# Kernel optimization log

Measured on AMD Instinct MI355X. Metric: run time of the kernel, lower is better.

## Reference

```python
import jax, jax.numpy as jnp
import numpy as np

N, C, H, W = 8, 192, 112, 112
TEMPERATURE = 0.1


def setup_inputs() -> dict:
    key = jax.random.key(0)
    k1, k2 = jax.random.split(key)
    features = jax.random.normal(k1, (N, C, H, W), dtype=jnp.float32)
    # Raw per-pixel directions in {-1, 0, 1}; clip the neighbor coordinate into
    # bounds and recompute the direction so EVERY neighbor is valid. The torch
    # module's broadcasting (labels[:, i, j] vs an (N, M) gather) only works when
    # all N neighbors are valid at each pixel, so this matches its assumptions.
    raw = jax.random.randint(k2, (N, 2, H, W), -1, 2)
    ii = jnp.arange(H)[None, :, None]
    jj = jnp.arange(W)[None, None, :]
    d0 = jnp.clip(ii + raw[:, 0], 0, H - 1) - ii
    d1 = jnp.clip(jj + raw[:, 1], 0, W - 1) - jj
    directions = jnp.stack([d0, d1], axis=1).astype(jnp.int32)
    # Single-class labels: the original loss is -inf whenever any mask entry is 0
    # (log of exactly 0), so a finite, comparable baseline needs matching labels.
    labels = jnp.zeros((N, H, W), dtype=jnp.int32)
    return {"features": features, "labels": labels, "directions": directions}


def reference(features, labels, directions):
    # F.normalize(features, dim=1): x / max(||x||_2, eps)
    norm = jnp.linalg.norm(features, axis=1, keepdims=True)
    fn = features / jnp.maximum(norm, 1e-12)

    ii = jnp.arange(H)[None, :, None]
    jj = jnp.arange(W)[None, None, :]
    ni = ii + directions[:, 0]  # (N, H, W), in-bounds by construction
    nj = jj + directions[:, 1]  # (N, H, W)

    # Torch: features[:, :, neighbor_i, neighbor_j] gathers the M(==N) neighbor
    # coordinates across ALL batch elements -> (N, C, N, H, W) = [n, c, m, i, j]
    gathered = fn[:, :, ni, nj]
    # logits[n, m, i, j] = <fn[n, :, i, j], fn[n, :, ni[m,i,j], nj[m,i,j]]> / T
    logits = jnp.einsum('ncij,ncmij->nmij', fn, gathered) / TEMPERATURE

    # mask[n, m, i, j] = (labels[m, i, j] == labels[n, ni[m,i,j], nj[m,i,j]])
    # (torch broadcasts labels[:, i, j] along the first axis of the (N, M) gather)
    labels_g = labels[:, ni, nj]  # (N, N, H, W) = [n, m, i, j]
    mask = (labels[None, :, :, :] == labels_g).astype(fn.dtype)

    exp_l = jnp.exp(logits) * mask
    denom = jnp.sum(exp_l, axis=1, keepdims=True)  # sum over m
    # sum_{i,j} mean_{n,m}(.) / (H*W) == global mean over (n, m, i, j)
    loss = (-jnp.log(exp_l / (denom + 1e-6))).mean()
    return loss
```

## Files before the change

### kernel.cpp

```cpp
#include <hip/hip_runtime.h>
#include <math.h>


namespace {
constexpr int N_ = 8, C_ = 192, H_ = 112, W_ = 112;
constexpr int HW = H_ * W_;
constexpr int TH = 2;
constexpr int WS = 56;
constexpr int TROWS = TH + 2;
constexpr int TCOLS = WS + 2;
constexpr int TILE_E = TROWS * TCOLS;
constexpr int NT = 128;
constexpr int NPX = TH * WS;
constexpr int EXTRA = TILE_E - NT;
constexpr int KCH = 8;
constexpr int GRP = KCH / 2;
constexpr int NCHUNK = C_ / KCH;
constexpr int NBLK = 2 * (H_ / TH) * N_;
constexpr float INV_T = 10.0f;
constexpr double TOTAL = (double)N_ * N_ * H_ * W_;
}

__device__ __forceinline__ float sel3(int d, float a, float b, float c) {
    float r = (d < 0) ? a : b;
    return (d > 0) ? c : r;
}

extern "C" __global__ void __launch_bounds__(NT, 4)
dcl_main(const float* __restrict__ feat,
         const int* __restrict__ labels,
         const int* __restrict__ dirs,
         double* __restrict__ partial, int use_partial)
{
    __shared__ float2 tiles[2][GRP][TILE_E];
    __shared__ float ssbuf[TILE_E];
    __shared__ float red[NT / 64];

    const int tid = threadIdx.x;
    const int gx0 = blockIdx.x * WS;
    const int gy0 = blockIdx.y * TH;
    const int n   = blockIdx.z;

    int gofs0, gofs1 = 0;
    {
        int r = tid / TCOLS, c = tid - r * TCOLS;
        gofs0 = min(max(gy0 + r - 1, 0), H_ - 1) * W_ + min(max(gx0 + c - 1, 0), W_ - 1);
        if (tid < EXTRA) {
            int t2 = tid + NT;
            r = t2 / TCOLS; c = t2 - r * TCOLS;
            gofs1 = min(max(gy0 + r - 1, 0), H_ - 1) * W_ + min(max(gx0 + c - 1, 0), W_ - 1);
        }
    }

    const bool is_px = (tid < NPX);
    const int ty = tid / WS;
    const int tx = tid - ty * WS;
    const int gi = gy0 + ty;
    const int gj = gx0 + tx;
    const int ci = (ty + 1) * TCOLS + (tx + 1);

    const float* __restrict__ plane = feat + (size_t)n * C_ * HW;

    float ss0 = 0.0f, ss1 = 0.0f;

    {
        #pragma unroll
        for (int g = 0; g < GRP; ++g) {
            float v0 = plane[(size_t)(2 * g) * HW + gofs0];
            float v1 = plane[(size_t)(2 * g + 1) * HW + gofs0];
            ss0 += v0 * v0 + v1 * v1;
            tiles[0][g][tid] = make_float2(v0, v1);
        }
        if (tid < EXTRA) {
            #pragma unroll
            for (int g = 0; g < GRP; ++g) {
                float u0 = plane[(size_t)(2 * g) * HW + gofs1];
                float u1 = plane[(size_t)(2 * g + 1) * HW + gofs1];
                ss1 += u0 * u0 + u1 * u1;
                tiles[0][g][tid + NT] = make_float2(u0, u1);
            }
        }
    }
    __syncthreads();

    float s[9];
    #pragma unroll
    for (int d = 0; d < 9; ++d) s[d] = 0.0f;

    for (int t = 0; t < NCHUNK; ++t) {
        float pv0[KCH], pv1[KCH];
        const bool more = (t + 1 < NCHUNK);
        if (more) {
            const float* p = plane + (size_t)(t + 1) * KCH * HW;
            #pragma unroll
            for (int k = 0; k < KCH; ++k) pv0[k] = p[(size_t)k * HW + gofs0];
            if (tid < EXTRA) {
                #pragma unroll
                for (int k = 0; k < KCH; ++k) pv1[k] = p[(size_t)k * HW + gofs1];
            }
        }

        if (is_px) {
            #pragma unroll
            for (int g = 0; g < GRP; ++g) {
                const float2* __restrict__ cp = tiles[t & 1][g];
                float2 fc  = cp[ci];
                float2 n00 = cp[ci - TCOLS - 1];
                float2 n01 = cp[ci - TCOLS];
                float2 n02 = cp[ci - TCOLS + 1];
                float2 n10 = cp[ci - 1];
                float2 n12 = cp[ci + 1];
                float2 n20 = cp[ci + TCOLS - 1];
                float2 n21 = cp[ci + TCOLS];
                float2 n22 = cp[ci + TCOLS + 1];
                s[0] = fmaf(fc.x, n00.x, s[0]); s[0] = fmaf(fc.y, n00.y, s[0]);
                s[1] = fmaf(fc.x, n01.x, s[1]); s[1] = fmaf(fc.y, n01.y, s[1]);
                s[2] = fmaf(fc.x, n02.x, s[2]); s[2] = fmaf(fc.y, n02.y, s[2]);
                s[3] = fmaf(fc.x, n10.x, s[3]); s[3] = fmaf(fc.y, n10.y, s[3]);
                s[4] = fmaf(fc.x, fc.x,  s[4]); s[4] = fmaf(fc.y, fc.y,  s[4]);
                s[5] = fmaf(fc.x, n12.x, s[5]); s[5] = fmaf(fc.y, n12.y, s[5]);
                s[6] = fmaf(fc.x, n20.x, s[6]); s[6] = fmaf(fc.y, n20.y, s[6]);
                s[7] = fmaf(fc.x, n21.x, s[7]); s[7] = fmaf(fc.y, n21.y, s[7]);
                s[8] = fmaf(fc.x, n22.x, s[8]); s[8] = fmaf(fc.y, n22.y, s[8]);
            }
        }

        if (more) {
            #pragma unroll
            for (int g = 0; g < GRP; ++g) {
                float v0 = pv0[2 * g], v1 = pv0[2 * g + 1];
                ss0 += v0 * v0 + v1 * v1;
                tiles[(t + 1) & 1][g][tid] = make_float2(v0, v1);
            }
            if (tid < EXTRA) {
                #pragma unroll
                for (int g = 0; g < GRP; ++g) {
                    float u0 = pv1[2 * g], u1 = pv1[2 * g + 1];
                    ss1 += u0 * u0 + u1 * u1;
                    tiles[(t + 1) & 1][g][tid + NT] = make_float2(u0, u1);
                }
            }
            __syncthreads();
        }
    }

    __syncthreads();
    ssbuf[tid] = 1.0f / fmaxf(sqrtf(ss0), 1e-12f);
    if (tid < EXTRA)
        ssbuf[tid + NT] = 1.0f / fmaxf(sqrtf(ss1), 1e-12f);
    __syncthreads();

    float lp = 0.0f;
    if (is_px) {
        const float invc = ssbuf[ci] * INV_T;
        const float l00 = s[0] * invc * ssbuf[ci - TCOLS - 1];
        const float l01 = s[1] * invc * ssbuf[ci - TCOLS];
        const float l02 = s[2] * invc * ssbuf[ci - TCOLS + 1];
        const float l10 = s[3] * invc * ssbuf[ci - 1];
        const float l11 = s[4] * invc * ssbuf[ci];
        const float l12 = s[5] * invc * ssbuf[ci + 1];
        const float l20 = s[6] * invc * ssbuf[ci + TCOLS - 1];
        const float l21 = s[7] * invc * ssbuf[ci + TCOLS];
        const float l22 = s[8] * invc * ssbuf[ci + TCOLS + 1];

        const int pix = gi * W_ + gj;
        float denom = 0.f, sumlog = 0.f;
        #pragma unroll
        for (int m = 0; m < N_; ++m) {
            int d0 = dirs[((m * 2 + 0) * H_ + gi) * W_ + gj];
            int d1 = dirs[((m * 2 + 1) * H_ + gi) * W_ + gj];
            float q0 = sel3(d1, l00, l01, l02);
            float q1 = sel3(d1, l10, l11, l12);
            float q2 = sel3(d1, l20, l21, l22);
            float lm = sel3(d0, q0, q1, q2);
            int labm = labels[m * HW + pix];
            int labn = labels[n * HW + (gi + d0) * W_ + (gj + d1)];
            bool msk = (labm == labn);
            float e = msk ? __expf(lm) : 0.f;
            denom += e;
            sumlog += msk ? lm : -INFINITY;
        }
        lp = 8.0f * __logf(denom + 1e-6f) - sumlog;
    }

    #pragma unroll
    for (int off = 32; off > 0; off >>= 1) lp += __shfl_down(lp, off, 64);
    const int wave = tid >> 6, lane = tid & 63;
    if (lane == 0) red[wave] = lp;
    __syncthreads();
    if (tid == 0) {
        const int bid = (blockIdx.z * gridDim.y + blockIdx.y) * gridDim.x + blockIdx.x;
        float t = red[0] + red[1];
        if (use_partial) partial[bid] = (double)t;
        else atomicAdd(partial, (double)t);
    }
}

extern "C" __global__ void __launch_bounds__(256)
dcl_final(const double* __restrict__ partial, float* __restrict__ out, int nblk)
{
    const int tid = threadIdx.x;
    double s = 0.0;
    for (int i = tid; i < nblk; i += 256) s += partial[i];
    #pragma unroll
    for (int off = 32; off > 0; off >>= 1) s += __shfl_down(s, off, 64);
    __shared__ double red[4];
    const int lane = tid & 63, wv = tid >> 6;
    if (lane == 0) red[wv] = s;
    __syncthreads();
    if (tid == 0) out[0] = (float)((red[0] + red[1] + red[2] + red[3]) / TOTAL);
}

extern "C" void kernel_launch(void* const* d_in, const int* in_sizes, int n_in,
                              void* d_out, int out_size, void* d_ws, size_t ws_size,
                              hipStream_t stream) {
    const float* feat   = (const float*)d_in[0];
    const int*   labels = (const int*)d_in[1];
    const int*   dirs   = (const int*)d_in[2];
    double* acc = (double*)d_ws;
    float*  out = (float*)d_out;

    const int use_partial = (ws_size >= (size_t)NBLK * sizeof(double)) ? 1 : 0;
    if (!use_partial) hipMemsetAsync(acc, 0, sizeof(double), stream);
    dim3 grid(2, H_ / TH, N_);
    dcl_main<<<grid, NT, 0, stream>>>(feat, labels, dirs, acc, use_partial);
    dcl_final<<<1, 256, 0, stream>>>(acc, out, use_partial ? NBLK : 1);
}
```

Before: 127.2 us.

## Split channels across two half-blocks, taller tiles, packed FMA dot products

```diff
diff --git a/kernel.cpp b/kernel.cpp
--- a/kernel.cpp
+++ b/kernel.cpp
@@ -5,20 +5,29 @@
 namespace {
 constexpr int N_ = 8, C_ = 192, H_ = 112, W_ = 112;
 constexpr int HW = H_ * W_;
-constexpr int TH = 2;
+constexpr int TH = 4;
 constexpr int WS = 56;
 constexpr int TROWS = TH + 2;
 constexpr int TCOLS = WS + 2;
 constexpr int TILE_E = TROWS * TCOLS;
-constexpr int NT = 128;
+constexpr int NT2 = 256;
+constexpr int NT = 2 * NT2;
 constexpr int NPX = TH * WS;
-constexpr int EXTRA = TILE_E - NT;
+constexpr int EXTRA = TILE_E - NT2;
+constexpr int CHALF = C_ / 2;
 constexpr int KCH = 8;
-constexpr int GRP = KCH / 2;
-constexpr int NCHUNK = C_ / KCH;
-constexpr int NBLK = 2 * (H_ / TH) * N_;
+constexpr int GRP = KCH / 4;
+constexpr int NCHUNK = CHALF / KCH;
+constexpr int NBLK = (W_ / WS) * (H_ / TH) * N_;
 constexpr float INV_T = 10.0f;
 constexpr double TOTAL = (double)N_ * N_ * H_ * W_;
+}
+
+typedef float v2f __attribute__((ext_vector_type(2)));
+typedef float v4f __attribute__((ext_vector_type(4)));
+
+__device__ __forceinline__ void pkfma(v2f& a, v2f x, v2f y) {
+    asm("v_pk_fma_f32 %0, %1, %2, %0" : "+v"(a) : "v"(x), "v"(y));
 }
 
 __device__ __forceinline__ float sel3(int d, float a, float b, float c) {
@@ -32,60 +41,72 @@
          const int* __restrict__ dirs,
          double* __restrict__ partial, int use_partial)
 {
-    __shared__ float2 tiles[2][GRP][TILE_E];
+    __shared__ v4f   tiles[2][2][GRP][TILE_E];
+    __shared__ float ssp[2][TILE_E];
     __shared__ float ssbuf[TILE_E];
+    __shared__ float scomb[NPX][9];
     __shared__ float red[NT / 64];
 
-    const int tid = threadIdx.x;
+    const int tid  = threadIdx.x;
+    const int half = tid >> 8;
+    const int t8   = tid & (NT2 - 1);
     const int gx0 = blockIdx.x * WS;
     const int gy0 = blockIdx.y * TH;
     const int n   = blockIdx.z;
 
     int gofs0, gofs1 = 0;
     {
-        int r = tid / TCOLS, c = tid - r * TCOLS;
+        int r = t8 / TCOLS, c = t8 - r * TCOLS;
         gofs0 = min(max(gy0 + r - 1, 0), H_ - 1) * W_ + min(max(gx0 + c - 1, 0), W_ - 1);
-        if (tid < EXTRA) {
-            int t2 = tid + NT;
+        if (t8 < EXTRA) {
+            int t2 = t8 + NT2;
             r = t2 / TCOLS; c = t2 - r * TCOLS;
             gofs1 = min(max(gy0 + r - 1, 0), H_ - 1) * W_ + min(max(gx0 + c - 1, 0), W_ - 1);
         }
     }
 
-    const bool is_px = (tid < NPX);
-    const int ty = tid / WS;
-    const int tx = tid - ty * WS;
+    const bool is_px = (t8 < NPX);
+    const int ty = t8 / WS;
+    const int tx = t8 - ty * WS;
     const int gi = gy0 + ty;
     const int gj = gx0 + tx;
     const int ci = (ty + 1) * TCOLS + (tx + 1);
 
-    const float* __restrict__ plane = feat + (size_t)n * C_ * HW;
+    const float* __restrict__ plane =
+        feat + ((size_t)n * C_ + (size_t)half * CHALF) * HW;
 
     float ss0 = 0.0f, ss1 = 0.0f;
 
     {
         #pragma unroll
         for (int g = 0; g < GRP; ++g) {
-            float v0 = plane[(size_t)(2 * g) * HW + gofs0];
-            float v1 = plane[(size_t)(2 * g + 1) * HW + gofs0];
-            ss0 += v0 * v0 + v1 * v1;
-            tiles[0][g][tid] = make_float2(v0, v1);
-        }
-        if (tid < EXTRA) {
+            float a0 = plane[(size_t)(4 * g + 0) * HW + gofs0];
+            float a1 = plane[(size_t)(4 * g + 1) * HW + gofs0];
+            float a2 = plane[(size_t)(4 * g + 2) * HW + gofs0];
+            float a3 = plane[(size_t)(4 * g + 3) * HW + gofs0];
+            ss0 += a0 * a0 + a1 * a1 + a2 * a2 + a3 * a3;
+            v4f v = {a0, a1, a2, a3};
+            tiles[half][0][g][t8] = v;
+        }
+        if (t8 < EXTRA) {
             #pragma unroll
             for (int g = 0; g < GRP; ++g) {
-                float u0 = plane[(size_t)(2 * g) * HW + gofs1];
-                float u1 = plane[(size_t)(2 * g + 1) * HW + gofs1];
-                ss1 += u0 * u0 + u1 * u1;
-                tiles[0][g][tid + NT] = make_float2(u0, u1);
-            }
-        }
-    }
-    __syncthreads();
-
-    float s[9];
+                float a0 = plane[(size_t)(4 * g + 0) * HW + gofs1];
+                float a1 = plane[(size_t)(4 * g + 1) * HW + gofs1];
+                float a2 = plane[(size_t)(4 * g + 2) * HW + gofs1];
+                float a3 = plane[(size_t)(4 * g + 3) * HW + gofs1];
+                ss1 += a0 * a0 + a1 * a1 + a2 * a2 + a3 * a3;
+                v4f v = {a0, a1, a2, a3};
+                tiles[half][0][g][t8 + NT2] = v;
+            }
+        }
+    }
+    __syncthreads();
+
+    v2f s2[9];
+    const v2f zero2 = {0.0f, 0.0f};
     #pragma unroll
-    for (int d = 0; d < 9; ++d) s[d] = 0.0f;
+    for (int d = 0; d < 9; ++d) s2[d] = zero2;
 
     for (int t = 0; t < NCHUNK; ++t) {
         float pv0[KCH], pv1[KCH];
@@ -94,7 +115,7 @@
             const float* p = plane + (size_t)(t + 1) * KCH * HW;
             #pragma unroll
             for (int k = 0; k < KCH; ++k) pv0[k] = p[(size_t)k * HW + gofs0];
-            if (tid < EXTRA) {
+            if (t8 < EXTRA) {
                 #pragma unroll
                 for (int k = 0; k < KCH; ++k) pv1[k] = p[(size_t)k * HW + gofs1];
             }
@@ -103,65 +124,90 @@
         if (is_px) {
             #pragma unroll
             for (int g = 0; g < GRP; ++g) {
-                const float2* __restrict__ cp = tiles[t & 1][g];
-                float2 fc  = cp[ci];
-                float2 n00 = cp[ci - TCOLS - 1];
-                float2 n01 = cp[ci - TCOLS];
-                float2 n02 = cp[ci - TCOLS + 1];
-                float2 n10 = cp[ci - 1];
-                float2 n12 = cp[ci + 1];
-                float2 n20 = cp[ci + TCOLS - 1];
-                float2 n21 = cp[ci + TCOLS];
-                float2 n22 = cp[ci + TCOLS + 1];
-                s[0] = fmaf(fc.x, n00.x, s[0]); s[0] = fmaf(fc.y, n00.y, s[0]);
-                s[1] = fmaf(fc.x, n01.x, s[1]); s[1] = fmaf(fc.y, n01.y, s[1]);
-                s[2] = fmaf(fc.x, n02.x, s[2]); s[2] = fmaf(fc.y, n02.y, s[2]);
-                s[3] = fmaf(fc.x, n10.x, s[3]); s[3] = fmaf(fc.y, n10.y, s[3]);
-                s[4] = fmaf(fc.x, fc.x,  s[4]); s[4] = fmaf(fc.y, fc.y,  s[4]);
-                s[5] = fmaf(fc.x, n12.x, s[5]); s[5] = fmaf(fc.y, n12.y, s[5]);
-                s[6] = fmaf(fc.x, n20.x, s[6]); s[6] = fmaf(fc.y, n20.y, s[6]);
-                s[7] = fmaf(fc.x, n21.x, s[7]); s[7] = fmaf(fc.y, n21.y, s[7]);
-                s[8] = fmaf(fc.x, n22.x, s[8]); s[8] = fmaf(fc.y, n22.y, s[8]);
+                const v4f* __restrict__ cp = tiles[half][t & 1][g];
+                v4f fc  = cp[ci];
+                v4f n00 = cp[ci - TCOLS - 1];
+                v4f n01 = cp[ci - TCOLS];
+                v4f n02 = cp[ci - TCOLS + 1];
+                v4f n10 = cp[ci - 1];
+                v4f n12 = cp[ci + 1];
+                v4f n20 = cp[ci + TCOLS - 1];
+                v4f n21 = cp[ci + TCOLS];
+                v4f n22 = cp[ci + TCOLS + 1];
+                pkfma(s2[0], fc.lo, n00.lo); pkfma(s2[0], fc.hi, n00.hi);
+                pkfma(s2[1], fc.lo, n01.lo); pkfma(s2[1], fc.hi, n01.hi);
+                pkfma(s2[2], fc.lo, n02.lo); pkfma(s2[2], fc.hi, n02.hi);
+                pkfma(s2[3], fc.lo, n10.lo); pkfma(s2[3], fc.hi, n10.hi);
+                pkfma(s2[5], fc.lo, n12.lo); pkfma(s2[5], fc.hi, n12.hi);
+                pkfma(s2[6], fc.lo, n20.lo); pkfma(s2[6], fc.hi, n20.hi);
+                pkfma(s2[7], fc.lo, n21.lo); pkfma(s2[7], fc.hi, n21.hi);
+                pkfma(s2[8], fc.lo, n22.lo); pkfma(s2[8], fc.hi, n22.hi);
             }
         }
 
         if (more) {
+            const int nb = (t + 1) & 1;
             #pragma unroll
             for (int g = 0; g < GRP; ++g) {
-                float v0 = pv0[2 * g], v1 = pv0[2 * g + 1];
-                ss0 += v0 * v0 + v1 * v1;
-                tiles[(t + 1) & 1][g][tid] = make_float2(v0, v1);
-            }
-            if (tid < EXTRA) {
+                float a0 = pv0[4 * g], a1 = pv0[4 * g + 1];
+                float a2 = pv0[4 * g + 2], a3 = pv0[4 * g + 3];
+                ss0 += a0 * a0 + a1 * a1 + a2 * a2 + a3 * a3;
+                v4f v = {a0, a1, a2, a3};
+                tiles[half][nb][g][t8] = v;
+            }
+            if (t8 < EXTRA) {
                 #pragma unroll
                 for (int g = 0; g < GRP; ++g) {
-                    float u0 = pv1[2 * g], u1 = pv1[2 * g + 1];
-                    ss1 += u0 * u0 + u1 * u1;
-                    tiles[(t + 1) & 1][g][tid + NT] = make_float2(u0, u1);
+                    float a0 = pv1[4 * g], a1 = pv1[4 * g + 1];
+                    float a2 = pv1[4 * g + 2], a3 = pv1[4 * g + 3];
+                    ss1 += a0 * a0 + a1 * a1 + a2 * a2 + a3 * a3;
+                    v4f v = {a0, a1, a2, a3};
+                    tiles[half][nb][g][t8 + NT2] = v;
                 }
             }
             __syncthreads();
         }
     }
 
-    __syncthreads();
-    ssbuf[tid] = 1.0f / fmaxf(sqrtf(ss0), 1e-12f);
-    if (tid < EXTRA)
-        ssbuf[tid + NT] = 1.0f / fmaxf(sqrtf(ss1), 1e-12f);
+    ssp[half][t8] = ss0;
+    if (t8 < EXTRA) ssp[half][t8 + NT2] = ss1;
+    if (half == 1 && is_px) {
+        scomb[t8][0] = s2[0].x + s2[0].y;
+        scomb[t8][1] = s2[1].x + s2[1].y;
+        scomb[t8][2] = s2[2].x + s2[2].y;
+        scomb[t8][3] = s2[3].x + s2[3].y;
+        scomb[t8][4] = s2[5].x + s2[5].y;
+        scomb[t8][5] = s2[6].x + s2[6].y;
+        scomb[t8][6] = s2[7].x + s2[7].y;
+        scomb[t8][7] = s2[8].x + s2[8].y;
+    }
+    __syncthreads();
+    if (tid < TILE_E)
+        ssbuf[tid] = 1.0f / fmaxf(sqrtf(ssp[0][tid] + ssp[1][tid]), 1e-12f);
     __syncthreads();
 
     float lp = 0.0f;
-    if (is_px) {
+    if (half == 0 && is_px) {
+        const float sA = s2[0].x + s2[0].y + scomb[t8][0];
+        const float sB = s2[1].x + s2[1].y + scomb[t8][1];
+        const float sC = s2[2].x + s2[2].y + scomb[t8][2];
+        const float sD = s2[3].x + s2[3].y + scomb[t8][3];
+        const float sE = s2[5].x + s2[5].y + scomb[t8][4];
+        const float sF = s2[6].x + s2[6].y + scomb[t8][5];
+        const float sG = s2[7].x + s2[7].y + scomb[t8][6];
+        const float sH = s2[8].x + s2[8].y + scomb[t8][7];
+        const float ssq = ssp[0][ci] + ssp[1][ci];
+
         const float invc = ssbuf[ci] * INV_T;
-        const float l00 = s[0] * invc * ssbuf[ci - TCOLS - 1];
-        const float l01 = s[1] * invc * ssbuf[ci - TCOLS];
-        const float l02 = s[2] * invc * ssbuf[ci - TCOLS + 1];
-        const float l10 = s[3] * invc * ssbuf[ci - 1];
-        const float l11 = s[4] * invc * ssbuf[ci];
-        const float l12 = s[5] * invc * ssbuf[ci + 1];
-        const float l20 = s[6] * invc * ssbuf[ci + TCOLS - 1];
-        const float l21 = s[7] * invc * ssbuf[ci + TCOLS];
-        const float l22 = s[8] * invc * ssbuf[ci + TCOLS + 1];
+        const float l00 = sA  * invc * ssbuf[ci - TCOLS - 1];
+        const float l01 = sB  * invc * ssbuf[ci - TCOLS];
+        const float l02 = sC  * invc * ssbuf[ci - TCOLS + 1];
+        const float l10 = sD  * invc * ssbuf[ci - 1];
+        const float l11 = ssq * invc * ssbuf[ci];
+        const float l12 = sE  * invc * ssbuf[ci + 1];
+        const float l20 = sF  * invc * ssbuf[ci + TCOLS - 1];
+        const float l21 = sG  * invc * ssbuf[ci + TCOLS];
+        const float l22 = sH  * invc * ssbuf[ci + TCOLS + 1];
 
         const int pix = gi * W_ + gj;
         float denom = 0.f, sumlog = 0.f;
@@ -189,10 +235,12 @@
     if (lane == 0) red[wave] = lp;
     __syncthreads();
     if (tid == 0) {
+        float tsum = 0.f;
+        #pragma unroll
+        for (int w = 0; w < NT / 64; ++w) tsum += red[w];
         const int bid = (blockIdx.z * gridDim.y + blockIdx.y) * gridDim.x + blockIdx.x;
-        float t = red[0] + red[1];
-        if (use_partial) partial[bid] = (double)t;
-        else atomicAdd(partial, (double)t);
+        if (use_partial) partial[bid] = (double)tsum;
+        else atomicAdd(partial, (double)tsum);
     }
 }
 
@@ -222,7 +270,7 @@
 
     const int use_partial = (ws_size >= (size_t)NBLK * sizeof(double)) ? 1 : 0;
     if (!use_partial) hipMemsetAsync(acc, 0, sizeof(double), stream);
-    dim3 grid(2, H_ / TH, N_);
+    dim3 grid(W_ / WS, H_ / TH, N_);
     dcl_main<<<grid, NT, 0, stream>>>(feat, labels, dirs, acc, use_partial);
     dcl_final<<<1, 256, 0, stream>>>(acc, out, use_partial ? NBLK : 1);
 }
```

Measured after the change: 119.2 us. 6.2% less time.

## Split channels across waves with 8x14 tiles, packed FMA and vertical pair reuse

Applied to the files above, without the earlier changes.

```diff
diff --git a/kernel.cpp b/kernel.cpp
--- a/kernel.cpp
+++ b/kernel.cpp
@@ -5,20 +5,29 @@
 namespace {
 constexpr int N_ = 8, C_ = 192, H_ = 112, W_ = 112;
 constexpr int HW = H_ * W_;
-constexpr int TH = 2;
-constexpr int WS = 56;
-constexpr int TROWS = TH + 2;
-constexpr int TCOLS = WS + 2;
-constexpr int TILE_E = TROWS * TCOLS;
-constexpr int NT = 128;
-constexpr int NPX = TH * WS;
-constexpr int EXTRA = TILE_E - NT;
+constexpr int TH = 8, WS = 14;
+constexpr int TCOLS = 16;
+constexpr int ROWP = 17;
+constexpr int NSLOT = 160;
+constexpr int NT = 256;
+constexpr int NPAIR = 4 * WS;
+constexpr int QCH = C_ / 4;
 constexpr int KCH = 8;
-constexpr int GRP = KCH / 2;
-constexpr int NCHUNK = C_ / KCH;
-constexpr int NBLK = 2 * (H_ / TH) * N_;
+constexpr int GRP = 2;
+constexpr int NCH = QCH / KCH;
+constexpr int NBLK = (H_ / TH) * (W_ / WS) * N_;
 constexpr float INV_T = 10.0f;
 constexpr double TOTAL = (double)N_ * N_ * H_ * W_;
+}
+
+typedef float v2f __attribute__((ext_vector_type(2)));
+typedef float v4f __attribute__((ext_vector_type(4)));
+
+__device__ __forceinline__ void pk(v2f& a, v2f x, v2f y) {
+    asm("v_pk_fma_f32 %0, %1, %2, %0" : "+v"(a) : "v"(x), "v"(y));
+}
+__device__ __forceinline__ void pk4(v2f& a, v4f x, v4f y) {
+    pk(a, x.lo, y.lo); pk(a, x.hi, y.hi);
 }
 
 __device__ __forceinline__ float sel3(int d, float a, float b, float c) {
@@ -26,153 +35,163 @@
     return (d > 0) ? c : r;
 }
 
-extern "C" __global__ void __launch_bounds__(NT, 4)
+extern "C" __global__ void __launch_bounds__(NT, 3)
 dcl_main(const float* __restrict__ feat,
          const int* __restrict__ labels,
          const int* __restrict__ dirs,
          double* __restrict__ partial, int use_partial)
 {
-    __shared__ float2 tiles[2][GRP][TILE_E];
-    __shared__ float ssbuf[TILE_E];
-    __shared__ float red[NT / 64];
-
-    const int tid = threadIdx.x;
-    const int gx0 = blockIdx.x * WS;
-    const int gy0 = blockIdx.y * TH;
-    const int n   = blockIdx.z;
-
-    int gofs0, gofs1 = 0;
+    __shared__ v4f   tilesA[4][GRP][10 * ROWP];
+    __shared__ float ssq[4][NSLOT];
+    __shared__ float ssbuf[NSLOT];
+    __shared__ float part[4][NPAIR][18];
+    __shared__ float red[4];
+
+    const int bid = blockIdx.x;
+    const int n   = bid & 7;
+    const int tt  = bid >> 3;
+    const int tyb = tt >> 3;
+    const int txb = tt & 7;
+    const int gy0 = tyb * TH;
+    const int gx0 = txb * WS;
+
+    const int tid  = threadIdx.x;
+    const int q    = tid >> 6;
+    const int lane = tid & 63;
+
+    const bool l32 = (lane < 32);
+    int li0, go0, li1, go1, li2 = 0, go2 = 0;
     {
-        int r = tid / TCOLS, c = tid - r * TCOLS;
-        gofs0 = min(max(gy0 + r - 1, 0), H_ - 1) * W_ + min(max(gx0 + c - 1, 0), W_ - 1);
-        if (tid < EXTRA) {
-            int t2 = tid + NT;
-            r = t2 / TCOLS; c = t2 - r * TCOLS;
-            gofs1 = min(max(gy0 + r - 1, 0), H_ - 1) * W_ + min(max(gx0 + c - 1, 0), W_ - 1);
-        }
-    }
-
-    const bool is_px = (tid < NPX);
-    const int ty = tid / WS;
-    const int tx = tid - ty * WS;
-    const int gi = gy0 + ty;
-    const int gj = gx0 + tx;
-    const int ci = (ty + 1) * TCOLS + (tx + 1);
-
-    const float* __restrict__ plane = feat + (size_t)n * C_ * HW;
-
-    float ss0 = 0.0f, ss1 = 0.0f;
-
+        int s = lane, r = s >> 4, c = s & 15;
+        li0 = r * ROWP + c;
+        go0 = min(max(gy0 + r - 1, 0), H_ - 1) * W_ + min(max(gx0 + c - 1, 0), W_ - 1);
+        s = lane + 64; r = s >> 4; c = s & 15;
+        li1 = r * ROWP + c;
+        go1 = min(max(gy0 + r - 1, 0), H_ - 1) * W_ + min(max(gx0 + c - 1, 0), W_ - 1);
+        if (l32) {
+            s = lane + 128; r = s >> 4; c = s & 15;
+            li2 = r * ROWP + c;
+            go2 = min(max(gy0 + r - 1, 0), H_ - 1) * W_ + min(max(gx0 + c - 1, 0), W_ - 1);
+        }
+    }
+
+    const bool is_pr = (lane < NPAIR);
+    const int pr = lane / WS;
+    const int tx = lane - pr * WS;
+    const int top = (2 * pr) * ROWP + tx;
+
+    const float* __restrict__ plane =
+        feat + ((size_t)n * C_ + (size_t)q * QCH) * HW;
+
+    float ss0 = 0.f, ss1 = 0.f, ss2 = 0.f;
+    float pva[KCH], pvb[KCH], pvc[KCH];
+
+    auto ld = [&](int go, int t, float* pv) {
+        const float* p = plane + (size_t)t * KCH * HW + go;
+        #pragma unroll
+        for (int k = 0; k < KCH; ++k) pv[k] = p[(size_t)k * HW];
+    };
+    auto wr = [&](int li, const float* pv, float& ss) {
+        ss += pv[0]*pv[0] + pv[1]*pv[1] + pv[2]*pv[2] + pv[3]*pv[3]
+            + pv[4]*pv[4] + pv[5]*pv[5] + pv[6]*pv[6] + pv[7]*pv[7];
+        v4f a = {pv[0], pv[1], pv[2], pv[3]};
+        v4f b = {pv[4], pv[5], pv[6], pv[7]};
+        tilesA[q][0][li] = a;
+        tilesA[q][1][li] = b;
+    };
+
+    ld(go0, 0, pva); ld(go1, 0, pvb); if (l32) ld(go2, 0, pvc);
+    wr(li0, pva, ss0); wr(li1, pvb, ss1); if (l32) wr(li2, pvc, ss2);
+
+    v2f q0[7], q1[7], s01;
     {
-        #pragma unroll
-        for (int g = 0; g < GRP; ++g) {
-            float v0 = plane[(size_t)(2 * g) * HW + gofs0];
-            float v1 = plane[(size_t)(2 * g + 1) * HW + gofs0];
-            ss0 += v0 * v0 + v1 * v1;
-            tiles[0][g][tid] = make_float2(v0, v1);
-        }
-        if (tid < EXTRA) {
+        const v2f z = {0.f, 0.f};
+        #pragma unroll
+        for (int d = 0; d < 7; ++d) { q0[d] = z; q1[d] = z; }
+        s01 = z;
+    }
+
+    for (int t = 0; t < NCH; ++t) {
+        const bool more = (t + 1 < NCH);
+        if (more) {
+            ld(go0, t + 1, pva); ld(go1, t + 1, pvb); if (l32) ld(go2, t + 1, pvc);
+        }
+        if (is_pr) {
             #pragma unroll
             for (int g = 0; g < GRP; ++g) {
-                float u0 = plane[(size_t)(2 * g) * HW + gofs1];
-                float u1 = plane[(size_t)(2 * g + 1) * HW + gofs1];
-                ss1 += u0 * u0 + u1 * u1;
-                tiles[0][g][tid + NT] = make_float2(u0, u1);
+                const v4f* __restrict__ cp = &tilesA[q][g][0];
+                v4f A0 = cp[top +  0], B0 = cp[top +  1], C0 = cp[top +  2];
+                v4f A1 = cp[top + 17], B1 = cp[top + 18], C1 = cp[top + 19];
+                v4f A2 = cp[top + 34], B2 = cp[top + 35], C2 = cp[top + 36];
+                pk4(q0[0], B1, A0); pk4(q0[1], B1, B0); pk4(q0[2], B1, C0);
+                pk4(q0[3], B1, A1); pk4(q0[4], B1, C1);
+                pk4(q0[5], B1, A2); pk4(s01,   B1, B2); pk4(q0[6], B1, C2);
+                v4f A3 = cp[top + 51], B3 = cp[top + 52], C3 = cp[top + 53];
+                pk4(q1[0], B2, A1); pk4(q1[1], B2, C1);
+                pk4(q1[2], B2, A2); pk4(q1[3], B2, C2);
+                pk4(q1[4], B2, A3); pk4(q1[5], B2, B3); pk4(q1[6], B2, C3);
             }
         }
-    }
-    __syncthreads();
-
-    float s[9];
-    #pragma unroll
-    for (int d = 0; d < 9; ++d) s[d] = 0.0f;
-
-    for (int t = 0; t < NCHUNK; ++t) {
-        float pv0[KCH], pv1[KCH];
-        const bool more = (t + 1 < NCHUNK);
         if (more) {
-            const float* p = plane + (size_t)(t + 1) * KCH * HW;
-            #pragma unroll
-            for (int k = 0; k < KCH; ++k) pv0[k] = p[(size_t)k * HW + gofs0];
-            if (tid < EXTRA) {
-                #pragma unroll
-                for (int k = 0; k < KCH; ++k) pv1[k] = p[(size_t)k * HW + gofs1];
-            }
-        }
-
-        if (is_px) {
-            #pragma unroll
-            for (int g = 0; g < GRP; ++g) {
-                const float2* __restrict__ cp = tiles[t & 1][g];
-                float2 fc  = cp[ci];
-                float2 n00 = cp[ci - TCOLS - 1];
-                float2 n01 = cp[ci - TCOLS];
-                float2 n02 = cp[ci - TCOLS + 1];
-                float2 n10 = cp[ci - 1];
-                float2 n12 = cp[ci + 1];
-                float2 n20 = cp[ci + TCOLS - 1];
-                float2 n21 = cp[ci + TCOLS];
-                float2 n22 = cp[ci + TCOLS + 1];
-                s[0] = fmaf(fc.x, n00.x, s[0]); s[0] = fmaf(fc.y, n00.y, s[0]);
-                s[1] = fmaf(fc.x, n01.x, s[1]); s[1] = fmaf(fc.y, n01.y, s[1]);
-                s[2] = fmaf(fc.x, n02.x, s[2]); s[2] = fmaf(fc.y, n02.y, s[2]);
-                s[3] = fmaf(fc.x, n10.x, s[3]); s[3] = fmaf(fc.y, n10.y, s[3]);
-                s[4] = fmaf(fc.x, fc.x,  s[4]); s[4] = fmaf(fc.y, fc.y,  s[4]);
-                s[5] = fmaf(fc.x, n12.x, s[5]); s[5] = fmaf(fc.y, n12.y, s[5]);
-                s[6] = fmaf(fc.x, n20.x, s[6]); s[6] = fmaf(fc.y, n20.y, s[6]);
-                s[7] = fmaf(fc.x, n21.x, s[7]); s[7] = fmaf(fc.y, n21.y, s[7]);
-                s[8] = fmaf(fc.x, n22.x, s[8]); s[8] = fmaf(fc.y, n22.y, s[8]);
-            }
-        }
-
-        if (more) {
-            #pragma unroll
-            for (int g = 0; g < GRP; ++g) {
-                float v0 = pv0[2 * g], v1 = pv0[2 * g + 1];
-                ss0 += v0 * v0 + v1 * v1;
-                tiles[(t + 1) & 1][g][tid] = make_float2(v0, v1);
-            }
-            if (tid < EXTRA) {
-                #pragma unroll
-                for (int g = 0; g < GRP; ++g) {
-                    float u0 = pv1[2 * g], u1 = pv1[2 * g + 1];
-                    ss1 += u0 * u0 + u1 * u1;
-                    tiles[(t + 1) & 1][g][tid + NT] = make_float2(u0, u1);
-                }
-            }
-            __syncthreads();
-        }
-    }
-
-    __syncthreads();
-    ssbuf[tid] = 1.0f / fmaxf(sqrtf(ss0), 1e-12f);
-    if (tid < EXTRA)
-        ssbuf[tid + NT] = 1.0f / fmaxf(sqrtf(ss1), 1e-12f);
+            wr(li0, pva, ss0); wr(li1, pvb, ss1); if (l32) wr(li2, pvc, ss2);
+        }
+    }
+
+    ssq[q][lane] = ss0;
+    ssq[q][lane + 64] = ss1;
+    if (l32) ssq[q][lane + 128] = ss2;
+    if (is_pr) {
+        float* d = part[q][lane];
+        d[0] = q0[0].x + q0[0].y;  d[1] = q0[1].x + q0[1].y;
+        d[2] = q0[2].x + q0[2].y;  d[3] = q0[3].x + q0[3].y;
+        d[4] = q0[4].x + q0[4].y;  d[5] = q0[5].x + q0[5].y;
+        d[6] = s01.x + s01.y;      d[7] = q0[6].x + q0[6].y;
+        d[8]  = q1[0].x + q1[0].y; d[9]  = s01.x + s01.y;
+        d[10] = q1[1].x + q1[1].y; d[11] = q1[2].x + q1[2].y;
+        d[12] = q1[3].x + q1[3].y; d[13] = q1[4].x + q1[4].y;
+        d[14] = q1[5].x + q1[5].y; d[15] = q1[6].x + q1[6].y;
+    }
+    __syncthreads();
+    if (tid < NSLOT)
+        ssbuf[tid] = 1.0f / fmaxf(
+            sqrtf(ssq[0][tid] + ssq[1][tid] + ssq[2][tid] + ssq[3][tid]), 1e-12f);
     __syncthreads();
 
     float lp = 0.0f;
-    if (is_px) {
-        const float invc = ssbuf[ci] * INV_T;
-        const float l00 = s[0] * invc * ssbuf[ci - TCOLS - 1];
-        const float l01 = s[1] * invc * ssbuf[ci - TCOLS];
-        const float l02 = s[2] * invc * ssbuf[ci - TCOLS + 1];
-        const float l10 = s[3] * invc * ssbuf[ci - 1];
-        const float l11 = s[4] * invc * ssbuf[ci];
-        const float l12 = s[5] * invc * ssbuf[ci + 1];
-        const float l20 = s[6] * invc * ssbuf[ci + TCOLS - 1];
-        const float l21 = s[7] * invc * ssbuf[ci + TCOLS];
-        const float l22 = s[8] * invc * ssbuf[ci + TCOLS + 1];
-
+    if (tid < TH * WS) {
+        const int er = tid / WS, ec = tid - (tid / WS) * WS;
+        const int lane_ = (er >> 1) * WS + ec;
+        const int off = (er & 1) * 8;
+        float f[8];
+        #pragma unroll
+        for (int k = 0; k < 8; ++k)
+            f[k] = part[0][lane_][off + k] + part[1][lane_][off + k]
+                 + part[2][lane_][off + k] + part[3][lane_][off + k];
+
+        const int ciu = (er + 1) * TCOLS + (ec + 1);
+        const float ssqc = ssq[0][ciu] + ssq[1][ciu] + ssq[2][ciu] + ssq[3][ciu];
+        const float invc = ssbuf[ciu] * INV_T;
+        const float l00 = f[0] * invc * ssbuf[ciu - TCOLS - 1];
+        const float l01 = f[1] * invc * ssbuf[ciu - TCOLS];
+        const float l02 = f[2] * invc * ssbuf[ciu - TCOLS + 1];
+        const float l10 = f[3] * invc * ssbuf[ciu - 1];
+        const float l11 = ssqc * invc * ssbuf[ciu];
+        const float l12 = f[4] * invc * ssbuf[ciu + 1];
+        const float l20 = f[5] * invc * ssbuf[ciu + TCOLS - 1];
+        const float l21 = f[6] * invc * ssbuf[ciu + TCOLS];
+        const float l22 = f[7] * invc * ssbuf[ciu + TCOLS + 1];
+
+        const int gi = gy0 + er, gj = gx0 + ec;
         const int pix = gi * W_ + gj;
         float denom = 0.f, sumlog = 0.f;
         #pragma unroll
         for (int m = 0; m < N_; ++m) {
             int d0 = dirs[((m * 2 + 0) * H_ + gi) * W_ + gj];
             int d1 = dirs[((m * 2 + 1) * H_ + gi) * W_ + gj];
-            float q0 = sel3(d1, l00, l01, l02);
-            float q1 = sel3(d1, l10, l11, l12);
-            float q2 = sel3(d1, l20, l21, l22);
-            float lm = sel3(d0, q0, q1, q2);
+            float e0 = sel3(d1, l00, l01, l02);
+            float e1 = sel3(d1, l10, l11, l12);
+            float e2 = sel3(d1, l20, l21, l22);
+            float lm = sel3(d0, e0, e1, e2);
             int labm = labels[m * HW + pix];
             int labn = labels[n * HW + (gi + d0) * W_ + (gj + d1)];
             bool msk = (labm == labn);
@@ -185,14 +204,13 @@
 
     #pragma unroll
     for (int off = 32; off > 0; off >>= 1) lp += __shfl_down(lp, off, 64);
-    const int wave = tid >> 6, lane = tid & 63;
-    if (lane == 0) red[wave] = lp;
+    const int wv = tid >> 6, ln = tid & 63;
+    if (ln == 0) red[wv] = lp;
     __syncthreads();
     if (tid == 0) {
-        const int bid = (blockIdx.z * gridDim.y + blockIdx.y) * gridDim.x + blockIdx.x;
-        float t = red[0] + red[1];
-        if (use_partial) partial[bid] = (double)t;
-        else atomicAdd(partial, (double)t);
+        float tsum = red[0] + red[1] + red[2] + red[3];
+        if (use_partial) partial[bid] = (double)tsum;
+        else atomicAdd(partial, (double)tsum);
     }
 }
 
@@ -222,7 +240,6 @@
 
     const int use_partial = (ws_size >= (size_t)NBLK * sizeof(double)) ? 1 : 0;
     if (!use_partial) hipMemsetAsync(acc, 0, sizeof(double), stream);
-    dim3 grid(2, H_ / TH, N_);
-    dcl_main<<<grid, NT, 0, stream>>>(feat, labels, dirs, acc, use_partial);
+    dcl_main<<<dim3(NBLK), NT, 0, stream>>>(feat, labels, dirs, acc, use_partial);
     dcl_final<<<1, 256, 0, stream>>>(acc, out, use_partial ? NBLK : 1);
 }
```

New measurement: 129.4 us. About the same (+1.8%).
